# Kernel optimization log

Hardware: AMD Instinct MI355X
Metric: run time of the kernel (lower is better)

Reference implementation:

```python
import jax, jax.numpy as jnp
import numpy as np

EPS = 1e-07
ORTH_LAMBDA = 0.1
KAMA = 1.0


def setup_inputs() -> dict:
    key = jax.random.key(0)
    ks = jax.random.split(key, 10)
    b, c, h, w, n = 8, 128, 128, 128, 16
    s = 0.05  # weight init scale
    return {
        "x":     jax.random.normal(ks[0], (b, c, h, w), jnp.float32),
        "Wsa":   jax.random.normal(ks[1], (c, c), jnp.float32) * s,
        "bsa":   jnp.zeros((c,), jnp.float32),
        "Wr":    jax.random.normal(ks[2], (c, c), jnp.float32) * s,
        "br":    jnp.zeros((c,), jnp.float32),
        "kn":    jax.random.normal(ks[3], (n, c), jnp.float32),  # (nClass, in_c, 1, 1) squeezed
        "Wo":    jax.random.normal(ks[4], (c, c), jnp.float32) * s,
        "bo":    jnp.zeros((c,), jnp.float32),
        "alpha": jnp.ones((1, n, 1), jnp.float32) * 0.1,
        "sigma": jnp.ones((1,), jnp.float32) * 0.5,  # torch inits 0; nonzero so out != x
    }


def reference(x, Wsa, bsa, Wr, br, kn, Wo, bo, alpha, sigma):
    b, c, h, w = x.shape
    n = kn.shape[0]
    hw = h * w

    conv1x1 = lambda W, bb: jnp.einsum('oc,bchw->bohw', W, x) + bb[:, None, None]
    xsa = conv1x1(Wsa, bsa)                       # (b,c,h,w)
    xr = conv1x1(Wr, br)                          # (b,c,h,w)
    xo = conv1x1(Wo, bo)                          # (b,c,h,w)
    xn = jnp.einsum('nc,bchw->bnhw', kn, x)       # (b,n,h,w), no bias

    # ---- orthogonality loss over class kernels ----
    sym = kn @ kn.T                               # (n,n)
    nrm = jnp.sqrt(jnp.sum(kn ** 2, axis=-1, keepdims=True))  # (n,1)
    loss = sym / (nrm @ nrm.T + EPS) - jnp.eye(n, dtype=x.dtype)
    orth_loss = ORTH_LAMBDA * jnp.log(jnp.sum(loss ** 2) + 1.0)

    xsa_r = xsa.reshape(b, c, hw)
    xr_r = xr.reshape(b, c, hw)
    xn_r = xn.reshape(b, n, hw)

    # ---- cosine-normalized class-channel relation ----
    relation = jnp.einsum('bnk,bck->bnc', xn_r, xr_r)            # (b,n,c)
    norm_xr = jnp.sqrt(jnp.sum(xr_r ** 2, axis=-1, keepdims=True))  # (b,c,1)
    norm_xn = jnp.sqrt(jnp.sum(xn_r ** 2, axis=-1, keepdims=True))  # (b,n,1)
    relation_norm = relation / (norm_xn @ jnp.swapaxes(norm_xr, 1, 2) + EPS)

    # ---- channel self-attention regularizer ----
    rela = jnp.einsum('bik,bjk->bij', xsa_r, xsa_r)              # (b,c,c)
    factor = rela * (1.0 - jnp.eye(c, dtype=x.dtype))
    regular = jax.nn.softmax(jnp.mean(factor, axis=1, keepdims=True), axis=-1)  # (b,1,c)

    alpha_c = jnp.clip(alpha, 0.0, 1.0)                          # (1,n,1)
    relation_norm = (relation_norm + alpha_c * regular) / KAMA
    att = jax.nn.softmax(relation_norm, axis=1)                  # (b,n,c)

    # ---- fused attention-weighted group norm (no (b,n,c,h,w) materialization)
    # hot_area[b,n,c,h,w] = xo[b,c,h,w] * att[b,n,c]; reductions over (c,h,w)
    s1 = jnp.sum(xo, axis=(2, 3))                                # (b,c) sum_hw xo
    s2 = jnp.sum(xo ** 2, axis=(2, 3))                           # (b,c) sum_hw xo^2
    cnt = jnp.sum(att, axis=2) * hw + EPS                        # (b,n)
    hot_sum = jnp.einsum('bnc,bc->bn', att, s1)                  # (b,n)
    fo_mean = hot_sum / cnt                                      # (b,n)
    sq = jnp.einsum('bnc,bc->bn', att ** 2, s2) - 2.0 * fo_mean * hot_sum \
         + (fo_mean ** 2) * (c * hw)
    fo_std = jnp.sqrt(sq / cnt)                                  # (b,n)

    # out[b,c,h,w] = sum_n (xo - mean)/(std+eps) * att = xo*A - B
    inv = 1.0 / (fo_std + EPS)                                   # (b,n)
    A = jnp.einsum('bnc,bn->bc', att, inv)                       # (b,c)
    B = jnp.einsum('bnc,bn->bc', att, fo_mean * inv)             # (b,c)
    out = x + sigma * (xo * A[:, :, None, None] - B[:, :, None, None])
    return out, orth_loss
```

## Files before the change

### kernel.cpp

```cpp
#include <hip/hip_runtime.h>
#include <hip/hip_bf16.h>

#define B_   8
#define C_   128
#define HW_  16384
#define N_   16
#define EPS_ 1e-7f

typedef unsigned short u16;
typedef __attribute__((ext_vector_type(8))) short s8v;
typedef __attribute__((ext_vector_type(4))) short s4v;
typedef __attribute__((ext_vector_type(4))) float f4v;

__device__ __forceinline__ u16 f2b(float f) {
  union { __hip_bfloat16 b; u16 u; } cv; cv.b = __float2bfloat16(f); return cv.u;
}
__device__ __forceinline__ float b2f(u16 u) {
  union { float f; unsigned int i; } cv; cv.i = ((unsigned int)u) << 16; return cv.f;
}
__device__ __forceinline__ float wredsum(float v) {
#pragma unroll
  for (int o = 32; o > 0; o >>= 1) v += __shfl_xor(v, o, 64);
  return v;
}
__device__ __forceinline__ float wredmax(float v) {
#pragma unroll
  for (int o = 32; o > 0; o >>= 1) v = fmaxf(v, __shfl_xor(v, o, 64));
  return v;
}

#define XS_ 132
__global__ __launch_bounds__(512, 4) void k_gram(
    const float* __restrict__ x, float* __restrict__ pbuf, float* __restrict__ psx,
    const float* __restrict__ Wsa, const float* __restrict__ kn,
    const float* __restrict__ Wo, float* __restrict__ u,
    float* __restrict__ loss_out, u16* __restrict__ wo_bf) {
  __shared__ u16 Xb[C_ * XS_];
  const int tid = threadIdx.x;
  const int b = blockIdx.y;

  if (blockIdx.x == 64) {
    if (b == 0) {
      if (tid < C_) {
        float s = 0.f;
        for (int i = 0; i < C_; ++i) s += Wsa[i * C_ + tid];
        u[tid] = s;
      }
    } else if (b == 1) {
      float* smf = (float*)Xb;
      const int i = tid >> 4, j = tid & 15;
      float s = 0.f;
      if (tid < 256) {
        for (int c = 0; c < C_; ++c) s += kn[i * C_ + c] * kn[j * C_ + c];
        if (i == j) smf[i] = sqrtf(s);
      }
      __syncthreads();
      float l2 = 0.f;
      if (tid < 256) {
        float l = s / (smf[i] * smf[j] + EPS_) - (i == j ? 1.f : 0.f);
        l2 = l * l;
      }
      float wv = wredsum(l2);
      if ((tid & 63) == 0) smf[16 + (tid >> 6)] = wv;
      __syncthreads();
      if (tid == 0) {
        float t = 0.f;
        for (int k = 0; k < 8; ++k) t += smf[16 + k];
        loss_out[0] = 0.1f * logf(t + 1.f);
      }
    } else if (b == 2) {
#pragma unroll
      for (int j = 0; j < 8; ++j) {
        int f = tid + 512 * j;
        float4 v = ((const float4*)Wo)[f];
        s4v s; s[0] = (short)f2b(v.x); s[1] = (short)f2b(v.y);
        s[2] = (short)f2b(v.z); s[3] = (short)f2b(v.w);
        ((s4v*)wo_bf)[f] = s;
      }
    }
    return;
  }

  const int p0 = blockIdx.x * 256;
  const int lane = tid & 63;
  const int w = tid >> 6;
  const int m = lane & 15, q = lane >> 4;
  const int rb = (w & 3) * 32, cb = (w >> 2) * 64;

  f4v acc[2][4];
#pragma unroll
  for (int a = 0; a < 2; ++a)
#pragma unroll
    for (int c2 = 0; c2 < 4; ++c2) acc[a][c2] = (f4v){0.f, 0.f, 0.f, 0.f};

  float sxp = 0.f;
  const float* xb = x + (size_t)b * C_ * HW_;
  const float* ro = xb + (size_t)(tid >> 5) * HW_ + p0 + 4 * (tid & 31);

  float4 v[8];
#pragma unroll
  for (int j = 0; j < 8; ++j) v[j] = *(const float4*)(ro + (size_t)(16 * j) * HW_);

#pragma unroll
  for (int t = 0; t < 2; ++t) {
#pragma unroll
    for (int j = 0; j < 8; ++j) {
      int c = (tid >> 5) + 16 * j;
      s4v s; s[0] = (short)f2b(v[j].x); s[1] = (short)f2b(v[j].y);
      s[2] = (short)f2b(v[j].z); s[3] = (short)f2b(v[j].w);
      *(s4v*)(&Xb[c * XS_ + 4 * (tid & 31)]) = s;
    }
    __syncthreads();
    if (t == 0) {
#pragma unroll
      for (int j = 0; j < 8; ++j) v[j] = *(const float4*)(ro + (size_t)(16 * j) * HW_ + 128);
    }
    if (tid < C_) {
#pragma unroll
      for (int kk = 0; kk < 16; ++kk) {
        s8v vv = *(const s8v*)(&Xb[tid * XS_ + 8 * kk]);
#pragma unroll
        for (int e = 0; e < 8; ++e) sxp += b2f((u16)vv[e]);
      }
    }
#pragma unroll
    for (int s = 0; s < 4; ++s) {
      const int k0 = 32 * s;
      s8v Af[2], Bf[4];
#pragma unroll
      for (int a = 0; a < 2; ++a)
        Af[a] = *(const s8v*)(&Xb[(rb + 16 * a + m) * XS_ + k0 + 8 * q]);
#pragma unroll
      for (int c2 = 0; c2 < 4; ++c2)
        Bf[c2] = *(const s8v*)(&Xb[(cb + 16 * c2 + m) * XS_ + k0 + 8 * q]);
#pragma unroll
      for (int a = 0; a < 2; ++a)
#pragma unroll
        for (int c2 = 0; c2 < 4; ++c2)
          acc[a][c2] = __builtin_amdgcn_mfma_f32_16x16x32_bf16(Af[a], Bf[c2], acc[a][c2], 0, 0, 0);
    }
    __syncthreads();
  }

  float* pg = pbuf + ((size_t)(blockIdx.x * B_ + b) << 14);
#pragma unroll
  for (int a = 0; a < 2; ++a)
#pragma unroll
    for (int c2 = 0; c2 < 4; ++c2)
#pragma unroll
      for (int r = 0; r < 4; ++r) {
        int row = rb + 16 * a + 4 * q + r;
        int col = cb + 16 * c2 + m;
        pg[row * C_ + col] = acc[a][c2][r];
      }
  if (tid < C_) psx[(blockIdx.x * B_ + b) * C_ + tid] = sxp;
}

__global__ __launch_bounds__(256) void k_greduce(const float4* __restrict__ pbuf4,
                                                 const float* __restrict__ psx,
                                                 float4* __restrict__ G4,
                                                 float* __restrict__ sx) {
  const int blk = blockIdx.x;
  if (blk < 128) {
    const int gid = blk * 256 + threadIdx.x;
    const int b = gid >> 12, idx4 = gid & 4095;
    float4 s = {0.f, 0.f, 0.f, 0.f};
#pragma unroll 16
    for (int ch = 0; ch < 64; ++ch) {
      float4 p = pbuf4[((size_t)(ch * B_ + b) << 12) + idx4];
      s.x += p.x; s.y += p.y; s.z += p.z; s.w += p.w;
    }
    G4[gid] = s;
  } else {
    const int tt = (blk - 128) * 256 + threadIdx.x;
    const int b = tt >> 7, c = tt & 127;
    float s = 0.f;
#pragma unroll 16
    for (int ch = 0; ch < 64; ++ch) s += psx[(ch * B_ + b) * C_ + c];
    sx[tt] = s;
  }
}

__global__ __launch_bounds__(64) void k_cols(
    const float* __restrict__ G, const float* __restrict__ sx,
    const float* __restrict__ Wr, const float* __restrict__ Wsa,
    const float* __restrict__ Wo, const float* __restrict__ kn,
    const float* __restrict__ u,
    float* diagR, float* diagSA, float* colsumSA, float* diagO,
    float* prv, float* psav, float* pov, float* rel, float* diagN, float* ksx) {
  const int b = blockIdx.y;
  const int col = blockIdx.x;
  const int lane = threadIdx.x;
  const float* Gb = G + b * C_ * C_;
  const float4* g0 = (const float4*)(Gb + lane * C_);
  const float4* g1 = (const float4*)(Gb + (64 + lane) * C_);
  const float sx0 = sx[b * C_ + lane], sx1 = sx[b * C_ + 64 + lane];

  if (col < C_) {
    const float4* wr = (const float4*)(Wr + col * C_);
    const float4* wa = (const float4*)(Wsa + col * C_);
    const float4* wo = (const float4*)(Wo + col * C_);
    float t0r = 0, t1r = 0, t0a = 0, t1a = 0, t0o = 0, t1o = 0;
    for (int c = 0; c < 32; ++c) {
      float4 a0 = g0[c], a1 = g1[c];
      float4 vr = wr[c], va = wa[c], vo = wo[c];
      t0r += a0.x * vr.x + a0.y * vr.y + a0.z * vr.z + a0.w * vr.w;
      t1r += a1.x * vr.x + a1.y * vr.y + a1.z * vr.z + a1.w * vr.w;
      t0a += a0.x * va.x + a0.y * va.y + a0.z * va.z + a0.w * va.w;
      t1a += a1.x * va.x + a1.y * va.y + a1.z * va.z + a1.w * va.w;
      t0o += a0.x * vo.x + a0.y * vo.y + a0.z * vo.z + a0.w * vo.w;
      t1o += a1.x * vo.x + a1.y * vo.y + a1.z * vo.z + a1.w * vo.w;
    }
    float wr0 = Wr[col * C_ + lane], wr1 = Wr[col * C_ + 64 + lane];
    float wa0 = Wsa[col * C_ + lane], wa1 = Wsa[col * C_ + 64 + lane];
    float wo0 = Wo[col * C_ + lane], wo1 = Wo[col * C_ + 64 + lane];
    float u0 = u[lane], u1 = u[64 + lane];
    float dR = wredsum(wr0 * t0r + wr1 * t1r);
    float pR = wredsum(wr0 * sx0 + wr1 * sx1);
    float dA = wredsum(wa0 * t0a + wa1 * t1a);
    float cA = wredsum(u0 * t0a + u1 * t1a);
    float pA = wredsum(wa0 * sx0 + wa1 * sx1);
    float dO = wredsum(wo0 * t0o + wo1 * t1o);
    float pO = wredsum(wo0 * sx0 + wo1 * sx1);
    float rl[N_];
#pragma unroll
    for (int n = 0; n < N_; ++n)
      rl[n] = wredsum(kn[n * C_ + lane] * t0r + kn[n * C_ + 64 + lane] * t1r);
    if (lane == 0) {
      diagR[b * C_ + col] = dR;  prv[b * C_ + col] = pR;
      diagSA[b * C_ + col] = dA; colsumSA[b * C_ + col] = cA; psav[b * C_ + col] = pA;
      diagO[b * C_ + col] = dO;  pov[b * C_ + col] = pO;
      for (int n = 0; n < N_; ++n) rel[(b * N_ + n) * C_ + col] = rl[n];
    }
  } else {
    const int n = col - C_;
    const float4* wk = (const float4*)(kn + n * C_);
    float t0 = 0, t1 = 0;
    for (int c = 0; c < 32; ++c) {
      float4 a0 = g0[c], a1 = g1[c], vk = wk[c];
      t0 += a0.x * vk.x + a0.y * vk.y + a0.z * vk.z + a0.w * vk.w;
      t1 += a1.x * vk.x + a1.y * vk.y + a1.z * vk.z + a1.w * vk.w;
    }
    float k0v = kn[n * C_ + lane], k1v = kn[n * C_ + 64 + lane];
    float dN = wredsum(k0v * t0 + k1v * t1);
    float kx = wredsum(k0v * sx0 + k1v * sx1);
    if (lane == 0) { diagN[b * N_ + n] = dN; ksx[b * N_ + n] = kx; }
  }
}

__global__ __launch_bounds__(128) void k_asm(
    const float* diagR, const float* diagSA, const float* colsumSA, const float* diagO,
    const float* prv, const float* psav, const float* pov,
    const float* rel, const float* diagN, const float* ksx,
    const float* br, const float* bo, const float* bsa, const float* alpha,
    float* Aout, float* Bout) {
  const int b = blockIdx.x;
  const int t = threadIdx.x;
  __shared__ float rb2[2];
  __shared__ float att_s[N_][C_ + 1];
  __shared__ float s1_s[C_], s2_s[C_];
  __shared__ float inv_s[N_], fmi_s[N_];
  const float hw = (float)HW_;
  const float bsa_c = bsa[t], br_c = br[t], bo_c = bo[t];
  const float psa_c = psav[b * C_ + t], pr_c = prv[b * C_ + t], po_c = pov[b * C_ + t];

  float bsum, psum, mx, ssum;
  { float wv = wredsum(bsa_c); if ((t & 63) == 0) rb2[t >> 6] = wv; __syncthreads();
    bsum = rb2[0] + rb2[1]; __syncthreads(); }
  { float wv = wredsum(psa_c); if ((t & 63) == 0) rb2[t >> 6] = wv; __syncthreads();
    psum = rb2[0] + rb2[1]; __syncthreads(); }

  const float nxr = sqrtf(fmaxf(diagR[b * C_ + t] + 2.f * br_c * pr_c + hw * br_c * br_c, 0.f));
  s1_s[t] = po_c + hw * bo_c;
  s2_s[t] = diagO[b * C_ + t] + 2.f * bo_c * po_c + hw * bo_c * bo_c;
  const float colsum = colsumSA[b * C_ + t] + bsum * psa_c + bsa_c * (psum + hw * bsum);
  const float diagv = diagSA[b * C_ + t] + 2.f * bsa_c * psa_c + hw * bsa_c * bsa_c;
  const float fm = (colsum - diagv) * (1.f / (float)C_);

  { float wv = wredmax(fm); if ((t & 63) == 0) rb2[t >> 6] = wv; __syncthreads();
    mx = fmaxf(rb2[0], rb2[1]); __syncthreads(); }
  const float ee = expf(fm - mx);
  { float wv = wredsum(ee); if ((t & 63) == 0) rb2[t >> 6] = wv; __syncthreads();
    ssum = rb2[0] + rb2[1]; __syncthreads(); }
  const float reg = ee / ssum;

  float r[N_];
  float rmax = -1e30f;
#pragma unroll
  for (int n = 0; n < N_; ++n) {
    float al = fminf(fmaxf(alpha[n], 0.f), 1.f);
    float nxn = sqrtf(fmaxf(diagN[b * N_ + n], 0.f));
    float rv = (rel[(b * N_ + n) * C_ + t] + br_c * ksx[b * N_ + n]) / (nxn * nxr + EPS_) + al * reg;
    r[n] = rv; rmax = fmaxf(rmax, rv);
  }
  float es = 0.f;
#pragma unroll
  for (int n = 0; n < N_; ++n) { r[n] = expf(r[n] - rmax); es += r[n]; }
  const float ies = 1.f / es;
#pragma unroll
  for (int n = 0; n < N_; ++n) att_s[n][t] = r[n] * ies;
  __syncthreads();

  if (t < N_) {
    float sa = 0.f, sh = 0.f, sq = 0.f;
    for (int c = 0; c < C_; ++c) {
      float a = att_s[t][c];
      sa += a; sh += a * s1_s[c]; sq += a * a * s2_s[c];
    }
    float cnt = sa * hw + EPS_;
    float fmean = sh / cnt;
    float sqv = sq - 2.f * fmean * sh + fmean * fmean * ((float)C_ * hw);
    float fstd = sqrtf(fmaxf(sqv, 0.f) / cnt);
    float inv = 1.f / (fstd + EPS_);
    inv_s[t] = inv; fmi_s[t] = fmean * inv;
  }
  __syncthreads();

  float Ac = 0.f, Bc = 0.f;
#pragma unroll
  for (int n = 0; n < N_; ++n) { float a = att_s[n][t]; Ac += a * inv_s[n]; Bc += a * fmi_s[n]; }
  Aout[b * C_ + t] = Ac; Bout[b * C_ + t] = Bc;
}

#define XT_ 132
__global__ __launch_bounds__(512, 4) void k_out(
    const float* __restrict__ x, const u16* __restrict__ wo_bf,
    const float* __restrict__ bo, const float* __restrict__ Aws,
    const float* __restrict__ Bws, const float* __restrict__ sig,
    float* __restrict__ out) {
  const int b = blockIdx.y;
  __shared__ u16 Xt[64 * XT_];
  __shared__ float As[C_], Bs[C_], bos[C_];
  const int tid = threadIdx.x, lane = tid & 63, w = tid >> 6;
  const int n = lane & 15, q = lane >> 4;

  if (tid < C_) { As[tid] = Aws[b * C_ + tid]; Bs[tid] = Bws[b * C_ + tid]; bos[tid] = bo[tid]; }
  const float sg = sig[0];

  s8v af[4];
#pragma unroll
  for (int s = 0; s < 4; ++s)
    af[s] = *(const s8v*)(wo_bf + (16 * w + n) * C_ + 32 * s + 8 * q);

  const float* xb = x + (size_t)b * C_ * HW_;
  float* ob = out + (size_t)b * C_ * HW_;
  const int pq = tid & 15;
  const int c4 = tid >> 4;

  float4 v[4];
  {
    const int p0 = blockIdx.x * 256;
    const float* src = xb + (size_t)(4 * c4) * HW_ + p0 + 4 * pq;
#pragma unroll
    for (int r2 = 0; r2 < 4; ++r2) v[r2] = *(const float4*)(src + (size_t)r2 * HW_);
  }

#pragma unroll 1
  for (int pt = 0; pt < 4; ++pt) {
    const int p0 = blockIdx.x * 256 + pt * 64;
    {
      float4 v0 = v[0], v1 = v[1], v2 = v[2], v3 = v[3];
      s4v s0, s1, s2, s3;
      s0[0] = (short)f2b(v0.x); s0[1] = (short)f2b(v1.x); s0[2] = (short)f2b(v2.x); s0[3] = (short)f2b(v3.x);
      s1[0] = (short)f2b(v0.y); s1[1] = (short)f2b(v1.y); s1[2] = (short)f2b(v2.y); s1[3] = (short)f2b(v3.y);
      s2[0] = (short)f2b(v0.z); s2[1] = (short)f2b(v1.z); s2[2] = (short)f2b(v2.z); s2[3] = (short)f2b(v3.z);
      s3[0] = (short)f2b(v0.w); s3[1] = (short)f2b(v1.w); s3[2] = (short)f2b(v2.w); s3[3] = (short)f2b(v3.w);
      *(s4v*)(&Xt[(4 * pq + 0) * XT_ + 4 * c4]) = s0;
      *(s4v*)(&Xt[(4 * pq + 1) * XT_ + 4 * c4]) = s1;
      *(s4v*)(&Xt[(4 * pq + 2) * XT_ + 4 * c4]) = s2;
      *(s4v*)(&Xt[(4 * pq + 3) * XT_ + 4 * c4]) = s3;
    }
    __syncthreads();
    if (pt < 3) {
      const float* src = xb + (size_t)(4 * c4) * HW_ + p0 + 64 + 4 * pq;
#pragma unroll
      for (int r2 = 0; r2 < 4; ++r2) v[r2] = *(const float4*)(src + (size_t)r2 * HW_);
    }

    f4v acc[4];
#pragma unroll
    for (int p2 = 0; p2 < 4; ++p2) acc[p2] = (f4v){0.f, 0.f, 0.f, 0.f};
#pragma unroll
    for (int s = 0; s < 4; ++s) {
#pragma unroll
      for (int p2 = 0; p2 < 4; ++p2) {
        s8v bfr = *(const s8v*)(&Xt[(16 * p2 + n) * XT_ + 32 * s + 8 * q]);
        acc[p2] = __builtin_amdgcn_mfma_f32_16x16x32_bf16(af[s], bfr, acc[p2], 0, 0, 0);
      }
    }

#pragma unroll
    for (int p2 = 0; p2 < 4; ++p2)
#pragma unroll
      for (int r = 0; r < 4; ++r) {
        int o = 16 * w + 4 * q + r;
        size_t idx = (size_t)o * HW_ + p0 + 16 * p2 + n;
        float xo = acc[p2][r] + bos[o];
        ob[idx] = xb[idx] + sg * (xo * As[o] - Bs[o]);
      }
    __syncthreads();
  }
}

extern "C" void kernel_launch(void* const* d_in, const int* in_sizes, int n_in,
                              void* d_out, int out_size, void* d_ws, size_t ws_size,
                              hipStream_t stream) {
  (void)in_sizes; (void)n_in; (void)out_size; (void)ws_size;
  const float* x     = (const float*)d_in[0];
  const float* Wsa   = (const float*)d_in[1];
  const float* bsa   = (const float*)d_in[2];
  const float* Wr    = (const float*)d_in[3];
  const float* br    = (const float*)d_in[4];
  const float* kn    = (const float*)d_in[5];
  const float* Wo    = (const float*)d_in[6];
  const float* bo    = (const float*)d_in[7];
  const float* alpha = (const float*)d_in[8];
  const float* sigma = (const float*)d_in[9];
  float* out = (float*)d_out;
  float* ws  = (float*)d_ws;

  float* G        = ws;
  float* sx       = ws + 131072;
  float* diagR    = ws + 132096;
  float* diagSA   = ws + 133120;
  float* colsumSA = ws + 134144;
  float* diagO    = ws + 135168;
  float* prv      = ws + 136192;
  float* psav     = ws + 137216;
  float* pov      = ws + 138240;
  float* rel      = ws + 139264;
  float* diagN    = ws + 155648;
  float* ksx      = ws + 155776;
  float* u        = ws + 155904;
  float* Aw       = ws + 156032;
  float* Bw       = ws + 157056;
  u16*   wo_bf    = (u16*)(ws + 158080);

  float* pbuf = out;
  float* psx  = out + 8388608;

  k_gram<<<dim3(65, 8), 512, 0, stream>>>(x, pbuf, psx, Wsa, kn, Wo, u,
      out + (size_t)B_ * C_ * HW_, wo_bf);
  k_greduce<<<132, 256, 0, stream>>>((const float4*)pbuf, psx, (float4*)G, sx);
  k_cols<<<dim3(144, 8), 64, 0, stream>>>(G, sx, Wr, Wsa, Wo, kn, u,
      diagR, diagSA, colsumSA, diagO, prv, psav, pov, rel, diagN, ksx);
  k_asm<<<8, 128, 0, stream>>>(diagR, diagSA, colsumSA, diagO, prv, psav, pov,
      rel, diagN, ksx, br, bo, bsa, alpha, Aw, Bw);
  k_out<<<dim3(64, 8), 512, 0, stream>>>(x, wo_bf, bo, Aw, Bw, sigma, out);
}
```

Before: 182.2 us.

## Use XOR-swizzled LDS tiles in gram and output kernels, retune reductions

The gram kernel now loads both 128-pixel halves up front into one 256-wide XOR-swizzled bf16 LDS tile, so it needs a single barrier and runs 8 MFMA k-steps instead of two staged passes. The channel sums are taken in fp32 with shuffle reductions instead of re-reading bf16 values from LDS. The output kernel processes 128-pixel tiles with 8 channels per thread and a swizzled 128x128 layout, halving the loop trips and barriers. k_greduce uses smaller blocks so more of them run, and k_asm's group-norm statistics are spread across all 128 threads with shuffle reductions instead of 16. The larger LDS footprints and higher register use may lower occupancy.

```diff
diff --git a/kernel.cpp b/kernel.cpp
--- a/kernel.cpp
+++ b/kernel.cpp
@@ -29,13 +29,13 @@
   return v;
 }
 
-#define XS_ 132
+#define XSB 512
 __global__ __launch_bounds__(512, 4) void k_gram(
     const float* __restrict__ x, float* __restrict__ pbuf, float* __restrict__ psx,
     const float* __restrict__ Wsa, const float* __restrict__ kn,
     const float* __restrict__ Wo, float* __restrict__ u,
     float* __restrict__ loss_out, u16* __restrict__ wo_bf) {
-  __shared__ u16 Xb[C_ * XS_];
+  __shared__ u16 Xb[C_ * 256];
   const int tid = threadIdx.x;
   const int b = blockIdx.y;
 
@@ -87,59 +87,69 @@
   const int m = lane & 15, q = lane >> 4;
   const int rb = (w & 3) * 32, cb = (w >> 2) * 64;
 
+  const float* xb = x + (size_t)b * C_ * HW_;
+  const int l32 = tid & 31;
+  const int rbase = tid >> 5;
+  const float* ro = xb + (size_t)rbase * HW_ + p0 + 4 * l32;
+  char* lds = (char*)Xb;
+
+  float4 v[8], v2[8];
+#pragma unroll
+  for (int j = 0; j < 8; ++j) v[j]  = *(const float4*)(ro + (size_t)(16 * j) * HW_);
+#pragma unroll
+  for (int j = 0; j < 8; ++j) v2[j] = *(const float4*)(ro + (size_t)(16 * j) * HW_ + 128);
+
+  const int swc = (rbase & 7) << 4;
+  float rs[8];
+#pragma unroll
+  for (int j = 0; j < 8; ++j) {
+    const int c = rbase + 16 * j;
+    s4v s; s[0] = (short)f2b(v[j].x); s[1] = (short)f2b(v[j].y);
+    s[2] = (short)f2b(v[j].z); s[3] = (short)f2b(v[j].w);
+    *(s4v*)(lds + c * XSB + ((8 * l32) ^ swc)) = s;
+    rs[j] = v[j].x + v[j].y + v[j].z + v[j].w;
+  }
+#pragma unroll
+  for (int j = 0; j < 8; ++j) {
+    const int c = rbase + 16 * j;
+    s4v s; s[0] = (short)f2b(v2[j].x); s[1] = (short)f2b(v2[j].y);
+    s[2] = (short)f2b(v2[j].z); s[3] = (short)f2b(v2[j].w);
+    *(s4v*)(lds + c * XSB + ((256 + 8 * l32) ^ swc)) = s;
+    rs[j] += v2[j].x + v2[j].y + v2[j].z + v2[j].w;
+  }
+#pragma unroll
+  for (int o = 16; o > 0; o >>= 1)
+#pragma unroll
+    for (int j = 0; j < 8; ++j) rs[j] += __shfl_xor(rs[j], o, 64);
+  if (l32 == 0) {
+#pragma unroll
+    for (int j = 0; j < 8; ++j)
+      psx[(blockIdx.x * B_ + b) * C_ + rbase + 16 * j] = rs[j];
+  }
+  __syncthreads();
+
   f4v acc[2][4];
 #pragma unroll
   for (int a = 0; a < 2; ++a)
 #pragma unroll
     for (int c2 = 0; c2 < 4; ++c2) acc[a][c2] = (f4v){0.f, 0.f, 0.f, 0.f};
 
-  float sxp = 0.f;
-  const float* xb = x + (size_t)b * C_ * HW_;
-  const float* ro = xb + (size_t)(tid >> 5) * HW_ + p0 + 4 * (tid & 31);
-
-  float4 v[8];
-#pragma unroll
-  for (int j = 0; j < 8; ++j) v[j] = *(const float4*)(ro + (size_t)(16 * j) * HW_);
-
-#pragma unroll
-  for (int t = 0; t < 2; ++t) {
-#pragma unroll
-    for (int j = 0; j < 8; ++j) {
-      int c = (tid >> 5) + 16 * j;
-      s4v s; s[0] = (short)f2b(v[j].x); s[1] = (short)f2b(v[j].y);
-      s[2] = (short)f2b(v[j].z); s[3] = (short)f2b(v[j].w);
-      *(s4v*)(&Xb[c * XS_ + 4 * (tid & 31)]) = s;
-    }
-    __syncthreads();
-    if (t == 0) {
-#pragma unroll
-      for (int j = 0; j < 8; ++j) v[j] = *(const float4*)(ro + (size_t)(16 * j) * HW_ + 128);
-    }
-    if (tid < C_) {
-#pragma unroll
-      for (int kk = 0; kk < 16; ++kk) {
-        s8v vv = *(const s8v*)(&Xb[tid * XS_ + 8 * kk]);
-#pragma unroll
-        for (int e = 0; e < 8; ++e) sxp += b2f((u16)vv[e]);
-      }
-    }
-#pragma unroll
-    for (int s = 0; s < 4; ++s) {
-      const int k0 = 32 * s;
-      s8v Af[2], Bf[4];
-#pragma unroll
-      for (int a = 0; a < 2; ++a)
-        Af[a] = *(const s8v*)(&Xb[(rb + 16 * a + m) * XS_ + k0 + 8 * q]);
+  const int swf = (m & 7) << 4;
+#pragma unroll
+  for (int s = 0; s < 8; ++s) {
+    const int off = (64 * s + 16 * q) ^ swf;
+    s8v Af[2], Bf[4];
+#pragma unroll
+    for (int a = 0; a < 2; ++a)
+      Af[a] = *(const s8v*)(lds + (rb + 16 * a + m) * XSB + off);
+#pragma unroll
+    for (int c2 = 0; c2 < 4; ++c2)
+      Bf[c2] = *(const s8v*)(lds + (cb + 16 * c2 + m) * XSB + off);
+#pragma unroll
+    for (int a = 0; a < 2; ++a)
 #pragma unroll
       for (int c2 = 0; c2 < 4; ++c2)
-        Bf[c2] = *(const s8v*)(&Xb[(cb + 16 * c2 + m) * XS_ + k0 + 8 * q]);
-#pragma unroll
-      for (int a = 0; a < 2; ++a)
-#pragma unroll
-        for (int c2 = 0; c2 < 4; ++c2)
-          acc[a][c2] = __builtin_amdgcn_mfma_f32_16x16x32_bf16(Af[a], Bf[c2], acc[a][c2], 0, 0, 0);
-    }
-    __syncthreads();
+        acc[a][c2] = __builtin_amdgcn_mfma_f32_16x16x32_bf16(Af[a], Bf[c2], acc[a][c2], 0, 0, 0);
   }
 
   float* pg = pbuf + ((size_t)(blockIdx.x * B_ + b) << 14);
@@ -153,16 +163,15 @@
         int col = cb + 16 * c2 + m;
         pg[row * C_ + col] = acc[a][c2][r];
       }
-  if (tid < C_) psx[(blockIdx.x * B_ + b) * C_ + tid] = sxp;
-}
-
-__global__ __launch_bounds__(256) void k_greduce(const float4* __restrict__ pbuf4,
+}
+
+__global__ __launch_bounds__(128) void k_greduce(const float4* __restrict__ pbuf4,
                                                  const float* __restrict__ psx,
                                                  float4* __restrict__ G4,
                                                  float* __restrict__ sx) {
   const int blk = blockIdx.x;
-  if (blk < 128) {
-    const int gid = blk * 256 + threadIdx.x;
+  if (blk < 256) {
+    const int gid = blk * 128 + threadIdx.x;
     const int b = gid >> 12, idx4 = gid & 4095;
     float4 s = {0.f, 0.f, 0.f, 0.f};
 #pragma unroll 16
@@ -172,7 +181,7 @@
     }
     G4[gid] = s;
   } else {
-    const int tt = (blk - 128) * 256 + threadIdx.x;
+    const int tt = (blk - 256) * 128 + threadIdx.x;
     const int b = tt >> 7, c = tt & 127;
     float s = 0.f;
 #pragma unroll 16
@@ -257,7 +266,7 @@
   const int b = blockIdx.x;
   const int t = threadIdx.x;
   __shared__ float rb2[2];
-  __shared__ float att_s[N_][C_ + 1];
+  __shared__ float att_s[C_][N_ + 1];
   __shared__ float s1_s[C_], s2_s[C_];
   __shared__ float inv_s[N_], fmi_s[N_];
   const float hw = (float)HW_;
@@ -298,38 +307,47 @@
   for (int n = 0; n < N_; ++n) { r[n] = expf(r[n] - rmax); es += r[n]; }
   const float ies = 1.f / es;
 #pragma unroll
-  for (int n = 0; n < N_; ++n) att_s[n][t] = r[n] * ies;
+  for (int n = 0; n < N_; ++n) att_s[t][n] = r[n] * ies;
   __syncthreads();
 
-  if (t < N_) {
+  {
+    const int nn = t >> 3, g = t & 7;
     float sa = 0.f, sh = 0.f, sq = 0.f;
-    for (int c = 0; c < C_; ++c) {
-      float a = att_s[t][c];
+#pragma unroll 4
+    for (int c = g; c < C_; c += 8) {
+      float a = att_s[c][nn];
       sa += a; sh += a * s1_s[c]; sq += a * a * s2_s[c];
     }
-    float cnt = sa * hw + EPS_;
-    float fmean = sh / cnt;
-    float sqv = sq - 2.f * fmean * sh + fmean * fmean * ((float)C_ * hw);
-    float fstd = sqrtf(fmaxf(sqv, 0.f) / cnt);
-    float inv = 1.f / (fstd + EPS_);
-    inv_s[t] = inv; fmi_s[t] = fmean * inv;
+#pragma unroll
+    for (int o = 4; o > 0; o >>= 1) {
+      sa += __shfl_xor(sa, o, 64);
+      sh += __shfl_xor(sh, o, 64);
+      sq += __shfl_xor(sq, o, 64);
+    }
+    if (g == 0) {
+      float cnt = sa * hw + EPS_;
+      float fmean = sh / cnt;
+      float sqv = sq - 2.f * fmean * sh + fmean * fmean * ((float)C_ * hw);
+      float fstd = sqrtf(fmaxf(sqv, 0.f) / cnt);
+      float inv = 1.f / (fstd + EPS_);
+      inv_s[nn] = inv; fmi_s[nn] = fmean * inv;
+    }
   }
   __syncthreads();
 
   float Ac = 0.f, Bc = 0.f;
 #pragma unroll
-  for (int n = 0; n < N_; ++n) { float a = att_s[n][t]; Ac += a * inv_s[n]; Bc += a * fmi_s[n]; }
+  for (int n = 0; n < N_; ++n) { float a = att_s[t][n]; Ac += a * inv_s[n]; Bc += a * fmi_s[n]; }
   Aout[b * C_ + t] = Ac; Bout[b * C_ + t] = Bc;
 }
 
-#define XT_ 132
 __global__ __launch_bounds__(512, 4) void k_out(
     const float* __restrict__ x, const u16* __restrict__ wo_bf,
     const float* __restrict__ bo, const float* __restrict__ Aws,
     const float* __restrict__ Bws, const float* __restrict__ sig,
     float* __restrict__ out) {
   const int b = blockIdx.y;
-  __shared__ u16 Xt[64 * XT_];
+  __shared__ u16 Xt[128 * 128];
   __shared__ float As[C_], Bs[C_], bos[C_];
   const int tid = threadIdx.x, lane = tid & 63, w = tid >> 6;
   const int n = lane & 15, q = lane >> 4;
@@ -344,61 +362,61 @@
 
   const float* xb = x + (size_t)b * C_ * HW_;
   float* ob = out + (size_t)b * C_ * HW_;
-  const int pq = tid & 15;
-  const int c4 = tid >> 4;
-
-  float4 v[4];
-  {
-    const int p0 = blockIdx.x * 256;
-    const float* src = xb + (size_t)(4 * c4) * HW_ + p0 + 4 * pq;
-#pragma unroll
-    for (int r2 = 0; r2 < 4; ++r2) v[r2] = *(const float4*)(src + (size_t)r2 * HW_);
-  }
+  const int pqd = tid & 31;
+  const int co  = tid >> 5;
+  const int p0 = blockIdx.x * 256;
+  char* lds = (char*)Xt;
+
+  float4 v[8];
+  const float* src0 = xb + (size_t)(8 * co) * HW_ + p0 + 4 * pqd;
+#pragma unroll
+  for (int r = 0; r < 8; ++r) v[r] = *(const float4*)(src0 + (size_t)r * HW_);
 
 #pragma unroll 1
-  for (int pt = 0; pt < 4; ++pt) {
-    const int p0 = blockIdx.x * 256 + pt * 64;
+  for (int pt = 0; pt < 2; ++pt) {
+    const int p = p0 + 128 * pt;
     {
-      float4 v0 = v[0], v1 = v[1], v2 = v[2], v3 = v[3];
-      s4v s0, s1, s2, s3;
-      s0[0] = (short)f2b(v0.x); s0[1] = (short)f2b(v1.x); s0[2] = (short)f2b(v2.x); s0[3] = (short)f2b(v3.x);
-      s1[0] = (short)f2b(v0.y); s1[1] = (short)f2b(v1.y); s1[2] = (short)f2b(v2.y); s1[3] = (short)f2b(v3.y);
-      s2[0] = (short)f2b(v0.z); s2[1] = (short)f2b(v1.z); s2[2] = (short)f2b(v2.z); s2[3] = (short)f2b(v3.z);
-      s3[0] = (short)f2b(v0.w); s3[1] = (short)f2b(v1.w); s3[2] = (short)f2b(v2.w); s3[3] = (short)f2b(v3.w);
-      *(s4v*)(&Xt[(4 * pq + 0) * XT_ + 4 * c4]) = s0;
-      *(s4v*)(&Xt[(4 * pq + 1) * XT_ + 4 * c4]) = s1;
-      *(s4v*)(&Xt[(4 * pq + 2) * XT_ + 4 * c4]) = s2;
-      *(s4v*)(&Xt[(4 * pq + 3) * XT_ + 4 * c4]) = s3;
+      const float* vf = (const float*)v;
+#pragma unroll
+      for (int pp = 0; pp < 4; ++pp) {
+        const int row = 4 * pqd + pp;
+        s8v s;
+#pragma unroll
+        for (int r = 0; r < 8; ++r) s[r] = (short)f2b(vf[4 * r + pp]);
+        *(s8v*)(lds + row * 256 + ((16 * co) ^ ((row & 7) << 4))) = s;
+      }
     }
     __syncthreads();
-    if (pt < 3) {
-      const float* src = xb + (size_t)(4 * c4) * HW_ + p0 + 64 + 4 * pq;
-#pragma unroll
-      for (int r2 = 0; r2 < 4; ++r2) v[r2] = *(const float4*)(src + (size_t)r2 * HW_);
-    }
-
-    f4v acc[4];
-#pragma unroll
-    for (int p2 = 0; p2 < 4; ++p2) acc[p2] = (f4v){0.f, 0.f, 0.f, 0.f};
+    if (pt == 0) {
+      const float* src1 = src0 + 128;
+#pragma unroll
+      for (int r = 0; r < 8; ++r) v[r] = *(const float4*)(src1 + (size_t)r * HW_);
+    }
+
+    f4v acc[8];
+#pragma unroll
+    for (int p2 = 0; p2 < 8; ++p2) acc[p2] = (f4v){0.f, 0.f, 0.f, 0.f};
 #pragma unroll
     for (int s = 0; s < 4; ++s) {
-#pragma unroll
-      for (int p2 = 0; p2 < 4; ++p2) {
-        s8v bfr = *(const s8v*)(&Xt[(16 * p2 + n) * XT_ + 32 * s + 8 * q]);
+      const int off = 64 * s + 16 * q;
+#pragma unroll
+      for (int p2 = 0; p2 < 8; ++p2) {
+        const int row = 16 * p2 + n;
+        s8v bfr = *(const s8v*)(lds + row * 256 + (off ^ ((row & 7) << 4)));
         acc[p2] = __builtin_amdgcn_mfma_f32_16x16x32_bf16(af[s], bfr, acc[p2], 0, 0, 0);
       }
     }
 
 #pragma unroll
-    for (int p2 = 0; p2 < 4; ++p2)
+    for (int p2 = 0; p2 < 8; ++p2)
 #pragma unroll
       for (int r = 0; r < 4; ++r) {
         int o = 16 * w + 4 * q + r;
-        size_t idx = (size_t)o * HW_ + p0 + 16 * p2 + n;
+        size_t idx = (size_t)o * HW_ + p + 16 * p2 + n;
         float xo = acc[p2][r] + bos[o];
         ob[idx] = xb[idx] + sg * (xo * As[o] - Bs[o]);
       }
-    __syncthreads();
+    if (pt == 0) __syncthreads();
   }
 }
 
@@ -441,7 +459,7 @@
 
   k_gram<<<dim3(65, 8), 512, 0, stream>>>(x, pbuf, psx, Wsa, kn, Wo, u,
       out + (size_t)B_ * C_ * HW_, wo_bf);
-  k_greduce<<<132, 256, 0, stream>>>((const float4*)pbuf, psx, (float4*)G, sx);
+  k_greduce<<<264, 128, 0, stream>>>((const float4*)pbuf, psx, (float4*)G, sx);
   k_cols<<<dim3(144, 8), 64, 0, stream>>>(G, sx, Wr, Wsa, Wo, kn, u,
       diagR, diagSA, colsumSA, diagO, prv, psav, pov, rel, diagN, ksx);
   k_asm<<<8, 128, 0, stream>>>(diagR, diagSA, colsumSA, diagO, prv, psav, pov,
```

After: 210.6 us. 1.16x slower.

## Coalesce gram partial stores, compute row sums in registers, fold affine epilogue constants

Applied to the files above, without the earlier changes.

The gram kernel now stores MFMA accumulators as nontemporal float4 vectors in fragment order, and the reduce kernel scatters them back to row-major. Per-channel sums are taken from the fp32 registers with shuffles instead of being re-read as bf16 from LDS, which also changes their precision to full fp32. k_asm spreads the per-class reductions over all threads and precomputes sigma*A and sigma*(A*bo-B), so the output epilogue becomes a single FMA with nontemporal load and store. The aim is to cut strided scalar stores, LDS work and epilogue arithmetic, at the cost of extra index math in the reduce kernel.

```diff
diff --git a/kernel.cpp b/kernel.cpp
--- a/kernel.cpp
+++ b/kernel.cpp
@@ -93,7 +93,6 @@
 #pragma unroll
     for (int c2 = 0; c2 < 4; ++c2) acc[a][c2] = (f4v){0.f, 0.f, 0.f, 0.f};
 
-  float sxp = 0.f;
   const float* xb = x + (size_t)b * C_ * HW_;
   const float* ro = xb + (size_t)(tid >> 5) * HW_ + p0 + 4 * (tid & 31);
 
@@ -101,6 +100,7 @@
 #pragma unroll
   for (int j = 0; j < 8; ++j) v[j] = *(const float4*)(ro + (size_t)(16 * j) * HW_);
 
+  float rs[8];
 #pragma unroll
   for (int t = 0; t < 2; ++t) {
 #pragma unroll
@@ -109,19 +109,13 @@
       s4v s; s[0] = (short)f2b(v[j].x); s[1] = (short)f2b(v[j].y);
       s[2] = (short)f2b(v[j].z); s[3] = (short)f2b(v[j].w);
       *(s4v*)(&Xb[c * XS_ + 4 * (tid & 31)]) = s;
+      float rsum = v[j].x + v[j].y + v[j].z + v[j].w;
+      if (t == 0) rs[j] = rsum; else rs[j] += rsum;
     }
     __syncthreads();
     if (t == 0) {
 #pragma unroll
       for (int j = 0; j < 8; ++j) v[j] = *(const float4*)(ro + (size_t)(16 * j) * HW_ + 128);
-    }
-    if (tid < C_) {
-#pragma unroll
-      for (int kk = 0; kk < 16; ++kk) {
-        s8v vv = *(const s8v*)(&Xb[tid * XS_ + 8 * kk]);
-#pragma unroll
-        for (int e = 0; e < 8; ++e) sxp += b2f((u16)vv[e]);
-      }
     }
 #pragma unroll
     for (int s = 0; s < 4; ++s) {
@@ -142,37 +136,46 @@
     __syncthreads();
   }
 
-  float* pg = pbuf + ((size_t)(blockIdx.x * B_ + b) << 14);
+  f4v* pg4 = (f4v*)pbuf + ((size_t)(blockIdx.x * B_ + b) << 12);
 #pragma unroll
   for (int a = 0; a < 2; ++a)
 #pragma unroll
     for (int c2 = 0; c2 < 4; ++c2)
-#pragma unroll
-      for (int r = 0; r < 4; ++r) {
-        int row = rb + 16 * a + 4 * q + r;
-        int col = cb + 16 * c2 + m;
-        pg[row * C_ + col] = acc[a][c2][r];
-      }
-  if (tid < C_) psx[(blockIdx.x * B_ + b) * C_ + tid] = sxp;
-}
-
-__global__ __launch_bounds__(256) void k_greduce(const float4* __restrict__ pbuf4,
+      __builtin_nontemporal_store(acc[a][c2], &pg4[(w * 8 + a * 4 + c2) * 64 + lane]);
+
+#pragma unroll
+  for (int o = 16; o > 0; o >>= 1)
+#pragma unroll
+    for (int j = 0; j < 8; ++j) rs[j] += __shfl_xor(rs[j], o, 64);
+  if ((tid & 31) == 0) {
+#pragma unroll
+    for (int j = 0; j < 8; ++j)
+      psx[(blockIdx.x * B_ + b) * C_ + (tid >> 5) + 16 * j] = rs[j];
+  }
+}
+
+__global__ __launch_bounds__(128) void k_greduce(const f4v* __restrict__ pbuf4,
                                                  const float* __restrict__ psx,
-                                                 float4* __restrict__ G4,
+                                                 float* __restrict__ G,
                                                  float* __restrict__ sx) {
   const int blk = blockIdx.x;
-  if (blk < 128) {
-    const int gid = blk * 256 + threadIdx.x;
-    const int b = gid >> 12, idx4 = gid & 4095;
-    float4 s = {0.f, 0.f, 0.f, 0.f};
+  if (blk < 256) {
+    const int gid = blk * 128 + threadIdx.x;
+    const int b = gid >> 12, i4 = gid & 4095;
+    f4v s = (f4v){0.f, 0.f, 0.f, 0.f};
 #pragma unroll 16
     for (int ch = 0; ch < 64; ++ch) {
-      float4 p = pbuf4[((size_t)(ch * B_ + b) << 12) + idx4];
-      s.x += p.x; s.y += p.y; s.z += p.z; s.w += p.w;
-    }
-    G4[gid] = s;
+      f4v p = __builtin_nontemporal_load(&pbuf4[((size_t)(ch * B_ + b) << 12) + i4]);
+      s += p;
+    }
+    const int w = i4 >> 9, j = (i4 >> 6) & 7, lane = i4 & 63;
+    const int a = j >> 2, c2 = j & 3, q = lane >> 4, m = lane & 15;
+    const int row0 = (w & 3) * 32 + 16 * a + 4 * q;
+    const int col = (w >> 2) * 64 + 16 * c2 + m;
+    float* Gp = G + b * C_ * C_ + row0 * C_ + col;
+    Gp[0] = s.x; Gp[C_] = s.y; Gp[2 * C_] = s.z; Gp[3 * C_] = s.w;
   } else {
-    const int tt = (blk - 128) * 256 + threadIdx.x;
+    const int tt = (blk - 256) * 128 + threadIdx.x;
     const int b = tt >> 7, c = tt & 127;
     float s = 0.f;
 #pragma unroll 16
@@ -253,11 +256,11 @@
     const float* prv, const float* psav, const float* pov,
     const float* rel, const float* diagN, const float* ksx,
     const float* br, const float* bo, const float* bsa, const float* alpha,
-    float* Aout, float* Bout) {
+    const float* sigma, float* C1out, float* C0out) {
   const int b = blockIdx.x;
   const int t = threadIdx.x;
   __shared__ float rb2[2];
-  __shared__ float att_s[N_][C_ + 1];
+  __shared__ float att_s[C_][N_ + 1];
   __shared__ float s1_s[C_], s2_s[C_];
   __shared__ float inv_s[N_], fmi_s[N_];
   const float hw = (float)HW_;
@@ -298,44 +301,54 @@
   for (int n = 0; n < N_; ++n) { r[n] = expf(r[n] - rmax); es += r[n]; }
   const float ies = 1.f / es;
 #pragma unroll
-  for (int n = 0; n < N_; ++n) att_s[n][t] = r[n] * ies;
+  for (int n = 0; n < N_; ++n) att_s[t][n] = r[n] * ies;
   __syncthreads();
 
-  if (t < N_) {
+  {
+    const int nn = t >> 3, g = t & 7;
     float sa = 0.f, sh = 0.f, sq = 0.f;
-    for (int c = 0; c < C_; ++c) {
-      float a = att_s[t][c];
+#pragma unroll 4
+    for (int c = g; c < C_; c += 8) {
+      float a = att_s[c][nn];
       sa += a; sh += a * s1_s[c]; sq += a * a * s2_s[c];
     }
-    float cnt = sa * hw + EPS_;
-    float fmean = sh / cnt;
-    float sqv = sq - 2.f * fmean * sh + fmean * fmean * ((float)C_ * hw);
-    float fstd = sqrtf(fmaxf(sqv, 0.f) / cnt);
-    float inv = 1.f / (fstd + EPS_);
-    inv_s[t] = inv; fmi_s[t] = fmean * inv;
+#pragma unroll
+    for (int o = 4; o > 0; o >>= 1) {
+      sa += __shfl_xor(sa, o, 64);
+      sh += __shfl_xor(sh, o, 64);
+      sq += __shfl_xor(sq, o, 64);
+    }
+    if (g == 0) {
+      float cnt = sa * hw + EPS_;
+      float fmean = sh / cnt;
+      float sqv = sq - 2.f * fmean * sh + fmean * fmean * ((float)C_ * hw);
+      float fstd = sqrtf(fmaxf(sqv, 0.f) / cnt);
+      float inv = 1.f / (fstd + EPS_);
+      inv_s[nn] = inv; fmi_s[nn] = fmean * inv;
+    }
   }
   __syncthreads();
 
   float Ac = 0.f, Bc = 0.f;
 #pragma unroll
-  for (int n = 0; n < N_; ++n) { float a = att_s[n][t]; Ac += a * inv_s[n]; Bc += a * fmi_s[n]; }
-  Aout[b * C_ + t] = Ac; Bout[b * C_ + t] = Bc;
+  for (int n = 0; n < N_; ++n) { float a = att_s[t][n]; Ac += a * inv_s[n]; Bc += a * fmi_s[n]; }
+  const float sg = sigma[0];
+  C1out[b * C_ + t] = sg * Ac;
+  C0out[b * C_ + t] = sg * (Ac * bo_c - Bc);
 }
 
 #define XT_ 132
 __global__ __launch_bounds__(512, 4) void k_out(
     const float* __restrict__ x, const u16* __restrict__ wo_bf,
-    const float* __restrict__ bo, const float* __restrict__ Aws,
-    const float* __restrict__ Bws, const float* __restrict__ sig,
+    const float* __restrict__ c1g, const float* __restrict__ c0g,
     float* __restrict__ out) {
   const int b = blockIdx.y;
   __shared__ u16 Xt[64 * XT_];
-  __shared__ float As[C_], Bs[C_], bos[C_];
+  __shared__ float c1s[C_], c0s[C_];
   const int tid = threadIdx.x, lane = tid & 63, w = tid >> 6;
   const int n = lane & 15, q = lane >> 4;
 
-  if (tid < C_) { As[tid] = Aws[b * C_ + tid]; Bs[tid] = Bws[b * C_ + tid]; bos[tid] = bo[tid]; }
-  const float sg = sig[0];
+  if (tid < C_) { c1s[tid] = c1g[b * C_ + tid]; c0s[tid] = c0g[b * C_ + tid]; }
 
   s8v af[4];
 #pragma unroll
@@ -395,8 +408,8 @@
       for (int r = 0; r < 4; ++r) {
         int o = 16 * w + 4 * q + r;
         size_t idx = (size_t)o * HW_ + p0 + 16 * p2 + n;
-        float xo = acc[p2][r] + bos[o];
-        ob[idx] = xb[idx] + sg * (xo * As[o] - Bs[o]);
+        float xv = __builtin_nontemporal_load(&xb[idx]);
+        __builtin_nontemporal_store(xv + c1s[o] * acc[p2][r] + c0s[o], &ob[idx]);
       }
     __syncthreads();
   }
@@ -432,8 +445,8 @@
   float* diagN    = ws + 155648;
   float* ksx      = ws + 155776;
   float* u        = ws + 155904;
-  float* Aw       = ws + 156032;
-  float* Bw       = ws + 157056;
+  float* C1w      = ws + 156032;
+  float* C0w      = ws + 157056;
   u16*   wo_bf    = (u16*)(ws + 158080);
 
   float* pbuf = out;
@@ -441,10 +454,10 @@
 
   k_gram<<<dim3(65, 8), 512, 0, stream>>>(x, pbuf, psx, Wsa, kn, Wo, u,
       out + (size_t)B_ * C_ * HW_, wo_bf);
-  k_greduce<<<132, 256, 0, stream>>>((const float4*)pbuf, psx, (float4*)G, sx);
+  k_greduce<<<264, 128, 0, stream>>>((const f4v*)pbuf, psx, G, sx);
   k_cols<<<dim3(144, 8), 64, 0, stream>>>(G, sx, Wr, Wsa, Wo, kn, u,
       diagR, diagSA, colsumSA, diagO, prv, psav, pov, rel, diagN, ksx);
   k_asm<<<8, 128, 0, stream>>>(diagR, diagSA, colsumSA, diagO, prv, psav, pov,
-      rel, diagN, ksx, br, bo, bsa, alpha, Aw, Bw);
-  k_out<<<dim3(64, 8), 512, 0, stream>>>(x, wo_bf, bo, Aw, Bw, sigma, out);
-}
+      rel, diagN, ksx, br, bo, bsa, alpha, sigma, C1w, C0w);
+  k_out<<<dim3(64, 8), 512, 0, stream>>>(x, wo_bf, C1w, C0w, out);
+}
```

New measurement: 195.3 us. 7.2% more time.
